# Kernel tuning notes

Measured on AMD Instinct MI355X. Metric: run time of the kernel, lower is better.

## Reference

```python
import jax, jax.numpy as jnp
import numpy as np

HIDDEN = 1024
HEADS = 16
HEAD = HIDDEN // HEADS


def setup_inputs() -> dict:
    key = jax.random.key(0)
    k1, k2, k3, k4, k5, k6 = jax.random.split(key, 6)
    B, S = 2, 2048
    x = jax.random.normal(k1, (B, S, HIDDEN), dtype=jnp.float32)
    mask = jax.random.randint(k2, (B, S), 0, 2, dtype=jnp.int32)
    # torch nn.Linear params: W [out,in], b [out]
    s = 1.0 / np.sqrt(HIDDEN)
    qkv_w = jax.random.uniform(k3, (3 * HIDDEN, HIDDEN), jnp.float32, -s, s)
    qkv_b = jax.random.uniform(k4, (3 * HIDDEN,), jnp.float32, -s, s)
    out_w = jax.random.uniform(k5, (HIDDEN, HIDDEN), jnp.float32, -s, s)
    out_b = jax.random.uniform(k6, (HIDDEN,), jnp.float32, -s, s)
    return {"x": x, "mask": mask, "qkv_w": qkv_w, "qkv_b": qkv_b,
            "out_w": out_w, "out_b": out_b}


def reference(x, mask, qkv_w, qkv_b, out_w, out_b):
    B, S, H = x.shape
    scale = HEAD ** -0.5
    qkv = x @ qkv_w.T + qkv_b                      # [B,S,3H]
    qkv = qkv.reshape(B, S, 3, HEADS, HEAD)
    qkv = jnp.transpose(qkv, (2, 0, 3, 1, 4))      # [3,B,h,S,d]
    q, k, v = qkv[0], qkv[1], qkv[2]
    scores = jnp.einsum('bhqd,bhkd->bhqk', q, k) * scale
    # key-padding mask [B,S] -> [B,1,1,S]
    scores = jnp.where(mask[:, None, None, :] == 0, -1e9, scores)
    attn = jax.nn.softmax(scores, axis=-1)
    # dropout is identity in eval mode
    ctx = jnp.einsum('bhqk,bhkd->bhqd', attn, v)   # [B,h,S,d]
    ctx = jnp.transpose(ctx, (0, 2, 1, 3)).reshape(B, S, H)
    return ctx @ out_w.T + out_b
```

## Files before the change

### kernel.cpp

```cpp
#include <hip/hip_runtime.h>
#include <hip/hip_bf16.h>

#define S_LEN 2048
#define NH    16
#define HD    64
#define HID   1024
#define BATCH 2
#define STK   72
#define SCQ   0.18033688f

typedef __bf16 bf16x8 __attribute__((ext_vector_type(8)));
typedef float  f32x4  __attribute__((ext_vector_type(4)));

__device__ __forceinline__ unsigned int pk2(float lo, float hi) {
    union { __hip_bfloat162 h; unsigned int u; } c;
    c.h = __float22bfloat162_rn(make_float2(lo, hi));
    return c.u;
}
__device__ __forceinline__ uint4 pk8(float4 a, float4 b) {
    uint4 o;
    o.x = pk2(a.x, a.y); o.y = pk2(a.z, a.w);
    o.z = pk2(b.x, b.y); o.w = pk2(b.z, b.w);
    return o;
}
__device__ __forceinline__ float exp2_hw(float x) {
    float r; asm("v_exp_f32 %0, %1" : "=v"(r) : "v"(x)); return r;
}
__device__ __forceinline__ void gll16(const unsigned short* g, unsigned short* l) {
    __builtin_amdgcn_global_load_lds(
        (const __attribute__((address_space(1))) void*)g,
        (__attribute__((address_space(3))) void*)l, 16, 0, 0);
}

__global__ __launch_bounds__(256)
void fill_constf(float* __restrict__ out, long n, float v) {
    long i = (long)blockIdx.x * 256 + threadIdx.x;
    const long stride = (long)gridDim.x * 256;
    for (; i < n; i += stride) out[i] = v;
}

__global__ __launch_bounds__(256)
void cvt_bf16(const float* __restrict__ src, unsigned short* __restrict__ dst, long n8) {
    long t = (long)blockIdx.x * 256 + threadIdx.x;
    const long stride = (long)gridDim.x * 256;
    for (; t < n8; t += stride) {
        const float4 a = *(const float4*)(src + t * 8);
        const float4 b = *(const float4*)(src + t * 8 + 4);
        *(uint4*)(dst + t * 8) = pk8(a, b);
    }
}
__global__ __launch_bounds__(256)
void cvt2_bf16(const float* __restrict__ s0, unsigned short* __restrict__ d0, long n0,
               const float* __restrict__ s1, unsigned short* __restrict__ d1, long n1) {
    long t = (long)blockIdx.x * 256 + threadIdx.x;
    const long stride = (long)gridDim.x * 256;
    for (; t < n0 + n1; t += stride) {
        const float* s; unsigned short* d; long i;
        if (t < n0) { s = s0; d = d0; i = t; } else { s = s1; d = d1; i = t - n0; }
        const float4 a = *(const float4*)(s + i * 8);
        const float4 b = *(const float4*)(s + i * 8 + 4);
        *(uint4*)(d + i * 8) = pk8(a, b);
    }
}

__global__ __launch_bounds__(256)
void gemm_bf16(const unsigned short* __restrict__ A,
               const unsigned short* __restrict__ W,
               const float* __restrict__ bias,
               unsigned short* __restrict__ o0,
               unsigned short* __restrict__ o1,
               unsigned short* __restrict__ o2,
               float* __restrict__ of,
               int mode)
{
    __shared__ __align__(16) unsigned short lA[3][128 * 32];
    __shared__ __align__(16) unsigned short lB[3][128 * 32];
    const int tid  = threadIdx.x;
    const int lane = tid & 63, wv = tid >> 6;
    const int quad = lane >> 4, l16 = lane & 15;
    const int wm = (wv & 1) * 64, wn = (wv >> 1) * 64;

    const int nwg = gridDim.x * gridDim.y;
    const int bid = blockIdx.y * gridDim.x + blockIdx.x;
    const int xcd = bid & 7, boff = bid >> 3;
    const int qd = nwg >> 3, rm = nwg & 7;
    const int swz = (xcd < rm ? xcd * (qd + 1) : rm * (qd + 1) + (xcd - rm) * qd) + boff;
    const int m0 = (swz / gridDim.x) * 128, n0 = (swz % gridDim.x) * 128;

    f32x4 acc[4][4] = {};

    const int srow0 = wv * 32 + (lane >> 2);
    const int srow1 = srow0 + 16;
    const int csrc  = ((lane & 3) ^ ((lane >> 3) & 3)) * 8;
    const unsigned short* pa0 = A + (long)(m0 + srow0) * HID + csrc;
    const unsigned short* pa1 = A + (long)(m0 + srow1) * HID + csrc;
    const unsigned short* pb0 = W + (long)(n0 + srow0) * HID + csrc;
    const unsigned short* pb1 = W + (long)(n0 + srow1) * HID + csrc;

    const int cq8 = (quad ^ ((l16 >> 1) & 3)) * 8;

#define STAGE_G(bufi, koff)                                        \
    do {                                                           \
        gll16(pa0 + (koff), &lA[bufi][(wv * 2 + 0) * 512]);        \
        gll16(pa1 + (koff), &lA[bufi][(wv * 2 + 1) * 512]);        \
        gll16(pb0 + (koff), &lB[bufi][(wv * 2 + 0) * 512]);        \
        gll16(pb1 + (koff), &lB[bufi][(wv * 2 + 1) * 512]);        \
    } while (0)

    STAGE_G(0, 0);
    STAGE_G(1, 32);

    int cur = 0;
    for (int k0 = 0; k0 < HID; k0 += 32) {
        if (k0 + 32 < HID) { asm volatile("s_waitcnt vmcnt(4)" ::: "memory"); }
        else               { asm volatile("s_waitcnt vmcnt(0)" ::: "memory"); }
        __builtin_amdgcn_s_barrier();
        asm volatile("" ::: "memory");

        if (k0 + 64 < HID) {
            const int nxt = cur ? cur - 1 : 2;
            STAGE_G(nxt, k0 + 64);
        }

        bf16x8 af[4], bfr[4];
#pragma unroll
        for (int mt = 0; mt < 4; mt++)
            af[mt] = *(const bf16x8*)&lA[cur][(wm + mt * 16 + l16) * 32 + cq8];
#pragma unroll
        for (int nt = 0; nt < 4; nt++)
            bfr[nt] = *(const bf16x8*)&lB[cur][(wn + nt * 16 + l16) * 32 + cq8];
#pragma unroll
        for (int mt = 0; mt < 4; mt++)
#pragma unroll
            for (int nt = 0; nt < 4; nt++)
                acc[mt][nt] = __builtin_amdgcn_mfma_f32_16x16x32_bf16(
                    af[mt], bfr[nt], acc[mt][nt], 0, 0, 0);

        cur = (cur < 2) ? cur + 1 : 0;
    }
#undef STAGE_G

    if (mode == 0) {
#pragma unroll
        for (int nt = 0; nt < 4; nt++) {
            const int n = n0 + wn + nt * 16 + l16;
            const float bv = bias[n];
            const int part = n >> 10, f = n & 1023, h = f >> 6, d = f & 63;
#pragma unroll
            for (int mt = 0; mt < 4; mt++) {
                const int mbase = m0 + wm + mt * 16 + quad * 4;
                const int b = mbase >> 11, s0 = mbase & 2047;
                const int bh = b * NH + h;
                if (part != 1) {
                    const float qsc = (part == 0) ? SCQ : 1.0f;
                    unsigned short* dst = (part == 0) ? o0 : o2;
                    uint2 o;
                    o.x = pk2((acc[mt][nt][0] + bv) * qsc, (acc[mt][nt][1] + bv) * qsc);
                    o.y = pk2((acc[mt][nt][2] + bv) * qsc, (acc[mt][nt][3] + bv) * qsc);
                    *(uint2*)&dst[((long)bh * HD + d) * S_LEN + s0] = o;
                } else {
#pragma unroll
                    for (int r = 0; r < 4; r++) {
                        union { __hip_bfloat16 h; unsigned short u; } cv;
                        cv.h = __float2bfloat16(acc[mt][nt][r] + bv);
                        o1[((long)bh * S_LEN + s0 + r) * HD + d] = cv.u;
                    }
                }
            }
        }
    } else {
#pragma unroll
        for (int nt = 0; nt < 4; nt++) {
            const int n = n0 + wn + nt * 16 + l16;
            const float bv = bias[n];
#pragma unroll
            for (int mt = 0; mt < 4; mt++) {
                const int mbase = m0 + wm + mt * 16 + quad * 4;
#pragma unroll
                for (int r = 0; r < 4; r++)
                    of[(long)(mbase + r) * HID + n] = acc[mt][nt][r] + bv;
            }
        }
    }
}

__global__ __launch_bounds__(512)
void attn(const unsigned short* __restrict__ q,
          const unsigned short* __restrict__ k,
          const unsigned short* __restrict__ vt_g,
          const int* __restrict__ mask,
          unsigned short* __restrict__ ctx)
{
    __shared__ __align__(16) unsigned short kt[2][64 * STK];
    __shared__ __align__(16) unsigned short vt[2][64 * STK];
    __shared__ __align__(16) __bf16 pt[8][16 * 72];
    __shared__ float mkv[2][64];

    const int tid  = threadIdx.x;
    const int lane = tid & 63, wv = tid >> 6;
    const int quad = lane >> 4, l16 = lane & 15;
    const int qt = blockIdx.x, h = blockIdx.y, b = blockIdx.z;
    const int bh = b * NH + h;

    const int sq = qt * 128 + wv * 16 + l16;

    const unsigned short* qtg = q + (long)bh * HD * S_LEN + sq;
    union { unsigned short u[8]; bf16x8 v; } qu0, qu1;
#pragma unroll
    for (int j = 0; j < 8; j++) {
        qu0.u[j] = qtg[(long)(quad * 8 + j) * S_LEN];
        qu1.u[j] = qtg[(long)(32 + quad * 8 + j) * S_LEN];
    }
    const bf16x8 qf0 = qu0.v, qf1 = qu1.v;

    float mrun = -1e30f;
    float lsum = 0.f;
    f32x4 Of[4] = {};

    const int sr = tid >> 3, sc8 = (tid & 7) * 8;
    const unsigned short* kg = k    + ((long)bh * S_LEN + sr) * HD + sc8;
    const unsigned short* vg = vt_g + ((long)bh * HD + sr) * S_LEN + sc8;
    __bf16* ptw = pt[wv];

    uint4 rk = *(const uint4*)(kg);
    uint4 rv = *(const uint4*)(vg);
    float rmv = 0.f;
    if (tid < 64) rmv = (mask[b * S_LEN + tid] == 0) ? -1e9f : 0.f;
    *(uint4*)&kt[0][sr * STK + sc8] = rk;
    *(uint4*)&vt[0][sr * STK + sc8] = rv;
    if (tid < 64) mkv[0][tid] = rmv;
    rk = *(const uint4*)(kg + (long)64 * HD);
    rv = *(const uint4*)(vg + 64);
    if (tid < 64) rmv = (mask[b * S_LEN + 64 + tid] == 0) ? -1e9f : 0.f;
    asm volatile("s_waitcnt lgkmcnt(0)" ::: "memory");
    __builtin_amdgcn_s_barrier();
    asm volatile("" ::: "memory");

    for (int k0 = 0; k0 < S_LEN; k0 += 64) {
        const int cur = (k0 >> 6) & 1;
        if (k0 + 64 < S_LEN) {
            *(uint4*)&kt[cur ^ 1][sr * STK + sc8] = rk;
            *(uint4*)&vt[cur ^ 1][sr * STK + sc8] = rv;
            if (tid < 64) mkv[cur ^ 1][tid] = rmv;
            if (k0 + 128 < S_LEN) {
                rk = *(const uint4*)(kg + (long)(k0 + 128) * HD);
                rv = *(const uint4*)(vg + (k0 + 128));
                if (tid < 64) rmv = (mask[b * S_LEN + k0 + 128 + tid] == 0) ? -1e9f : 0.f;
            }
        }

        float st[4][4];
        __builtin_amdgcn_s_setprio(1);
#pragma unroll
        for (int nt = 0; nt < 4; nt++) {
            bf16x8 k0f = *(const bf16x8*)&kt[cur][(nt * 16 + l16) * STK + quad * 8];
            bf16x8 k1f = *(const bf16x8*)&kt[cur][(nt * 16 + l16) * STK + 32 + quad * 8];
            const float4 mv = *(const float4*)&mkv[cur][nt * 16 + quad * 4];
            f32x4 s = {mv.x, mv.y, mv.z, mv.w};
            s = __builtin_amdgcn_mfma_f32_16x16x32_bf16(k0f, qf0, s, 0, 0, 0);
            s = __builtin_amdgcn_mfma_f32_16x16x32_bf16(k1f, qf1, s, 0, 0, 0);
#pragma unroll
            for (int r = 0; r < 4; r++) st[nt][r] = s[r];
        }
        __builtin_amdgcn_s_setprio(0);

        float mxa[4];
#pragma unroll
        for (int nt = 0; nt < 4; nt++)
            mxa[nt] = fmaxf(fmaxf(st[nt][0], st[nt][1]), fmaxf(st[nt][2], st[nt][3]));
        const float pmax = fmaxf(fmaxf(mxa[0], mxa[1]), fmaxf(mxa[2], mxa[3]));

        if (__any(pmax > mrun + 8.f)) {
            float mx = fmaxf(pmax, __shfl_xor(pmax, 16, 64));
            mx = fmaxf(mx, __shfl_xor(mx, 32, 64));
            const float mn = fmaxf(mrun, mx);
            const float alpha = exp2_hw(mrun - mn);
#pragma unroll
            for (int nt = 0; nt < 4; nt++) Of[nt] *= alpha;
            lsum *= alpha;
            mrun = mn;
        }

        float pr[4][4];
#pragma unroll
        for (int nt = 0; nt < 4; nt++)
#pragma unroll
            for (int r = 0; r < 4; r++) pr[nt][r] = exp2_hw(st[nt][r] - mrun);
        float rsa[4];
#pragma unroll
        for (int nt = 0; nt < 4; nt++)
            rsa[nt] = (pr[nt][0] + pr[nt][1]) + (pr[nt][2] + pr[nt][3]);
        lsum += (rsa[0] + rsa[1]) + (rsa[2] + rsa[3]);

#pragma unroll
        for (int nt = 0; nt < 4; nt++) {
            const unsigned long long lo = pk2(pr[nt][0], pr[nt][1]);
            const unsigned long long hi = pk2(pr[nt][2], pr[nt][3]);
            *(unsigned long long*)&ptw[l16 * 72 + nt * 16 + quad * 4] = lo | (hi << 32);
        }
        asm volatile("" ::: "memory");

        __builtin_amdgcn_s_setprio(1);
#pragma unroll
        for (int ks = 0; ks < 2; ks++) {
            bf16x8 bp = *(const bf16x8*)&ptw[l16 * 72 + ks * 32 + quad * 8];
#pragma unroll
            for (int nt = 0; nt < 4; nt++) {
                bf16x8 av = *(const bf16x8*)&vt[cur][(nt * 16 + l16) * STK + ks * 32 + quad * 8];
                Of[nt] = __builtin_amdgcn_mfma_f32_16x16x32_bf16(av, bp, Of[nt], 0, 0, 0);
            }
        }
        __builtin_amdgcn_s_setprio(0);

        asm volatile("s_waitcnt lgkmcnt(0)" ::: "memory");
        __builtin_amdgcn_s_barrier();
        asm volatile("" ::: "memory");
    }

    float lt = lsum + __shfl_xor(lsum, 16, 64);
    lt += __shfl_xor(lt, 32, 64);
    const float inv = 1.f / lt;
#pragma unroll
    for (int nt = 0; nt < 4; nt++) {
        uint2 o;
        o.x = pk2(Of[nt][0] * inv, Of[nt][1] * inv);
        o.y = pk2(Of[nt][2] * inv, Of[nt][3] * inv);
        *(uint2*)&ctx[((long)b * S_LEN + sq) * HID + h * HD + nt * 16 + quad * 4] = o;
    }
}

extern "C" void kernel_launch(void* const* d_in, const int* in_sizes, int n_in,
                              void* d_out, int out_size, void* d_ws, size_t ws_size,
                              hipStream_t stream) {
    float* outp = (float*)d_out;

    const float* x = nullptr; const int* mask = nullptr;
    const float* qkv_w = nullptr; const float* qkv_b = nullptr;
    const float* out_w = nullptr; const float* out_b = nullptr;
    for (int i = 0; i < n_in; i++) {
        switch (in_sizes[i]) {
            case 4194304: x     = (const float*)d_in[i]; break;
            case 4096:    mask  = (const int*)d_in[i];   break;
            case 3145728: qkv_w = (const float*)d_in[i]; break;
            case 3072:    qkv_b = (const float*)d_in[i]; break;
            case 1048576: out_w = (const float*)d_in[i]; break;
            case 1024:    out_b = (const float*)d_in[i]; break;
            default: break;
        }
    }
    if (!x || !mask || !qkv_w || !qkv_b || !out_w || !out_b) {
        fill_constf<<<256, 256, 0, stream>>>(outp, (long)out_size, 1000.0f);
        return;
    }

    const size_t per = (size_t)BATCH * NH * S_LEN * HD;
    const size_t nx  = (size_t)BATCH * S_LEN * HID;
    const size_t nqw = (size_t)3 * HID * HID;
    const size_t now = (size_t)HID * HID;
    if (ws_size < 4 * per * sizeof(unsigned short)) {
        fill_constf<<<256, 256, 0, stream>>>(outp, (long)out_size, 2000.0f);
        return;
    }

    unsigned short* wsq = (unsigned short*)d_ws;
    unsigned short* wsk = wsq + per;
    unsigned short* wsv = wsk + per;
    unsigned short* wsc = wsv + per;
    unsigned short* xb  = wsc;
    unsigned short* qwb = (unsigned short*)d_out;
    unsigned short* owb = wsq;

    cvt2_bf16<<<1024, 256, 0, stream>>>(x, xb, (long)(nx / 8), qkv_w, qwb, (long)(nqw / 8));
    gemm_bf16<<<dim3(3 * HID / 128, BATCH * S_LEN / 128), 256, 0, stream>>>(
        xb, qwb, qkv_b, wsq, wsk, wsv, nullptr, 0);
    attn<<<dim3(S_LEN / 128, NH, BATCH), 512, 0, stream>>>(wsq, wsk, wsv, mask, wsc);
    cvt_bf16<<<512, 256, 0, stream>>>(out_w, owb, (long)(now / 8));
    gemm_bf16<<<dim3(HID / 128, BATCH * S_LEN / 128), 256, 0, stream>>>(
        wsc, owb, out_b, nullptr, nullptr, nullptr, outp, 1);
}
```

Before: 225.5 us.

## Switch attention to 32x32x16 MFMA with register-resident P via permlane32 swap

Rewrites the attention kernel so each of four waves handles 32 queries using 32x32x16 bf16 MFMAs instead of 16x16x32 tiles. The softmax probabilities are repacked into MFMA operand layout in registers with permlane32_swap, which removes the per-wave LDS staging buffer for P and its write/read round trip. K/V tiles in LDS are XOR-swizzled to avoid bank conflicts, and block size drops from 512 to 256 threads. The trade-off is fewer waves per block and higher register pressure from the 16-wide accumulators, with more work per wave.

```diff
diff --git a/kernel.cpp b/kernel.cpp
--- a/kernel.cpp
+++ b/kernel.cpp
@@ -11,6 +11,8 @@
 
 typedef __bf16 bf16x8 __attribute__((ext_vector_type(8)));
 typedef float  f32x4  __attribute__((ext_vector_type(4)));
+typedef float  f32x16 __attribute__((ext_vector_type(16)));
+typedef unsigned u32x2 __attribute__((ext_vector_type(2)));
 
 __device__ __forceinline__ unsigned int pk2(float lo, float hi) {
     union { __hip_bfloat162 h; unsigned int u; } c;
@@ -25,6 +27,20 @@
 }
 __device__ __forceinline__ float exp2_hw(float x) {
     float r; asm("v_exp_f32 %0, %1" : "=v"(r) : "v"(x)); return r;
+}
+__device__ __forceinline__ void pl32swap(unsigned &a, unsigned &b) {
+    u32x2 r = __builtin_amdgcn_permlane32_swap(a, b, false, false);
+    a = r[0]; b = r[1];
+}
+__device__ __forceinline__ float pair_max(float x) {
+    unsigned u = __float_as_uint(x);
+    u32x2 r = __builtin_amdgcn_permlane32_swap(u, u, false, false);
+    return fmaxf(__uint_as_float(r[0]), __uint_as_float(r[1]));
+}
+__device__ __forceinline__ float pair_sum(float x) {
+    unsigned u = __float_as_uint(x);
+    u32x2 r = __builtin_amdgcn_permlane32_swap(u, u, false, false);
+    return __uint_as_float(r[0]) + __uint_as_float(r[1]);
 }
 __device__ __forceinline__ void gll16(const unsigned short* g, unsigned short* l) {
     __builtin_amdgcn_global_load_lds(
@@ -184,7 +200,7 @@
     }
 }
 
-__global__ __launch_bounds__(512)
+__global__ __launch_bounds__(256)
 void attn(const unsigned short* __restrict__ q,
           const unsigned short* __restrict__ k,
           const unsigned short* __restrict__ vt_g,
@@ -193,44 +209,48 @@
 {
     __shared__ __align__(16) unsigned short kt[2][64 * STK];
     __shared__ __align__(16) unsigned short vt[2][64 * STK];
-    __shared__ __align__(16) __bf16 pt[8][16 * 72];
-    __shared__ float mkv[2][64];
+    __shared__ __align__(16) float mkv[2][64];
 
     const int tid  = threadIdx.x;
     const int lane = tid & 63, wv = tid >> 6;
-    const int quad = lane >> 4, l16 = lane & 15;
+    const int ar = lane & 31, hi = lane >> 5;
     const int qt = blockIdx.x, h = blockIdx.y, b = blockIdx.z;
     const int bh = b * NH + h;
-
-    const int sq = qt * 128 + wv * 16 + l16;
-
-    const unsigned short* qtg = q + (long)bh * HD * S_LEN + sq;
-    union { unsigned short u[8]; bf16x8 v; } qu0, qu1;
-#pragma unroll
-    for (int j = 0; j < 8; j++) {
-        qu0.u[j] = qtg[(long)(quad * 8 + j) * S_LEN];
-        qu1.u[j] = qtg[(long)(32 + quad * 8 + j) * S_LEN];
-    }
-    const bf16x8 qf0 = qu0.v, qf1 = qu1.v;
-
-    float mrun = -1e30f;
-    float lsum = 0.f;
-    f32x4 Of[4] = {};
-
-    const int sr = tid >> 3, sc8 = (tid & 7) * 8;
-    const unsigned short* kg = k    + ((long)bh * S_LEN + sr) * HD + sc8;
-    const unsigned short* vg = vt_g + ((long)bh * HD + sr) * S_LEN + sc8;
-    __bf16* ptw = pt[wv];
-
-    uint4 rk = *(const uint4*)(kg);
-    uint4 rv = *(const uint4*)(vg);
+    const int sq = qt * 128 + wv * 32 + ar;
+
+    union { unsigned short u[8]; bf16x8 v; } qu[4];
+    const unsigned short* qg = q + (long)bh * HD * S_LEN + sq;
+#pragma unroll
+    for (int t = 0; t < 4; t++)
+#pragma unroll
+        for (int j = 0; j < 8; j++)
+            qu[t].u[j] = qg[(long)(16 * t + 8 * hi + j) * S_LEN];
+
+    float mrun = -1e30f, lsum = 0.f;
+    f32x16 Of0 = {}, Of1 = {};
+
+    const int sr = tid >> 2, c0 = tid & 3;
+    const unsigned short* kg = k    + ((long)bh * S_LEN + sr) * HD + c0 * 8;
+    const unsigned short* vg = vt_g + ((long)bh * HD + sr) * S_LEN + c0 * 8;
+    const int wof0 = sr * STK + ((c0 ^ (sr & 7)) * 8);
+    const int wof1 = sr * STK + (((c0 + 4) ^ (sr & 7)) * 8);
+    const int swzr = ar & 7;
+
+    uint4 rk0 = *(const uint4*)(kg);
+    uint4 rk1 = *(const uint4*)(kg + 32);
+    uint4 rv0 = *(const uint4*)(vg);
+    uint4 rv1 = *(const uint4*)(vg + 32);
     float rmv = 0.f;
     if (tid < 64) rmv = (mask[b * S_LEN + tid] == 0) ? -1e9f : 0.f;
-    *(uint4*)&kt[0][sr * STK + sc8] = rk;
-    *(uint4*)&vt[0][sr * STK + sc8] = rv;
+    *(uint4*)&kt[0][wof0] = rk0;
+    *(uint4*)&kt[0][wof1] = rk1;
+    *(uint4*)&vt[0][wof0] = rv0;
+    *(uint4*)&vt[0][wof1] = rv1;
     if (tid < 64) mkv[0][tid] = rmv;
-    rk = *(const uint4*)(kg + (long)64 * HD);
-    rv = *(const uint4*)(vg + 64);
+    rk0 = *(const uint4*)(kg + (long)64 * HD);
+    rk1 = *(const uint4*)(kg + (long)64 * HD + 32);
+    rv0 = *(const uint4*)(vg + 64);
+    rv1 = *(const uint4*)(vg + 64 + 32);
     if (tid < 64) rmv = (mask[b * S_LEN + 64 + tid] == 0) ? -1e9f : 0.f;
     asm volatile("s_waitcnt lgkmcnt(0)" ::: "memory");
     __builtin_amdgcn_s_barrier();
@@ -239,76 +259,93 @@
     for (int k0 = 0; k0 < S_LEN; k0 += 64) {
         const int cur = (k0 >> 6) & 1;
         if (k0 + 64 < S_LEN) {
-            *(uint4*)&kt[cur ^ 1][sr * STK + sc8] = rk;
-            *(uint4*)&vt[cur ^ 1][sr * STK + sc8] = rv;
+            *(uint4*)&kt[cur ^ 1][wof0] = rk0;
+            *(uint4*)&kt[cur ^ 1][wof1] = rk1;
+            *(uint4*)&vt[cur ^ 1][wof0] = rv0;
+            *(uint4*)&vt[cur ^ 1][wof1] = rv1;
             if (tid < 64) mkv[cur ^ 1][tid] = rmv;
             if (k0 + 128 < S_LEN) {
-                rk = *(const uint4*)(kg + (long)(k0 + 128) * HD);
-                rv = *(const uint4*)(vg + (k0 + 128));
+                rk0 = *(const uint4*)(kg + (long)(k0 + 128) * HD);
+                rk1 = *(const uint4*)(kg + (long)(k0 + 128) * HD + 32);
+                rv0 = *(const uint4*)(vg + (k0 + 128));
+                rv1 = *(const uint4*)(vg + (k0 + 128) + 32);
                 if (tid < 64) rmv = (mask[b * S_LEN + k0 + 128 + tid] == 0) ? -1e9f : 0.f;
             }
         }
 
-        float st[4][4];
+        float st[2][16];
         __builtin_amdgcn_s_setprio(1);
 #pragma unroll
-        for (int nt = 0; nt < 4; nt++) {
-            bf16x8 k0f = *(const bf16x8*)&kt[cur][(nt * 16 + l16) * STK + quad * 8];
-            bf16x8 k1f = *(const bf16x8*)&kt[cur][(nt * 16 + l16) * STK + 32 + quad * 8];
-            const float4 mv = *(const float4*)&mkv[cur][nt * 16 + quad * 4];
-            f32x4 s = {mv.x, mv.y, mv.z, mv.w};
-            s = __builtin_amdgcn_mfma_f32_16x16x32_bf16(k0f, qf0, s, 0, 0, 0);
-            s = __builtin_amdgcn_mfma_f32_16x16x32_bf16(k1f, qf1, s, 0, 0, 0);
-#pragma unroll
-            for (int r = 0; r < 4; r++) st[nt][r] = s[r];
+        for (int G = 0; G < 2; G++) {
+            f32x16 s = {};
+#pragma unroll
+            for (int t = 0; t < 4; t++) {
+                bf16x8 kf = *(const bf16x8*)
+                    &kt[cur][(G * 32 + ar) * STK + (((2 * t + hi) ^ swzr) * 8)];
+                s = __builtin_amdgcn_mfma_f32_32x32x16_bf16(kf, qu[t].v, s, 0, 0, 0);
+            }
+#pragma unroll
+            for (int m = 0; m < 4; m++) {
+                const float4 mv = *(const float4*)&mkv[cur][G * 32 + m * 8 + hi * 4];
+#pragma unroll
+                for (int r2 = 0; r2 < 4; r2++)
+                    st[G][m * 4 + r2] = s[m * 4 + r2] + (&mv.x)[r2];
+            }
         }
         __builtin_amdgcn_s_setprio(0);
 
-        float mxa[4];
-#pragma unroll
-        for (int nt = 0; nt < 4; nt++)
-            mxa[nt] = fmaxf(fmaxf(st[nt][0], st[nt][1]), fmaxf(st[nt][2], st[nt][3]));
-        const float pmax = fmaxf(fmaxf(mxa[0], mxa[1]), fmaxf(mxa[2], mxa[3]));
+        float pmax = st[0][0];
+#pragma unroll
+        for (int G = 0; G < 2; G++)
+#pragma unroll
+            for (int r = 0; r < 16; r++) pmax = fmaxf(pmax, st[G][r]);
+        pmax = pair_max(pmax);
 
         if (__any(pmax > mrun + 8.f)) {
-            float mx = fmaxf(pmax, __shfl_xor(pmax, 16, 64));
-            mx = fmaxf(mx, __shfl_xor(mx, 32, 64));
-            const float mn = fmaxf(mrun, mx);
+            const float mn = fmaxf(mrun, pmax);
             const float alpha = exp2_hw(mrun - mn);
-#pragma unroll
-            for (int nt = 0; nt < 4; nt++) Of[nt] *= alpha;
-            lsum *= alpha;
+            Of0 *= alpha; Of1 *= alpha; lsum *= alpha;
             mrun = mn;
         }
 
-        float pr[4][4];
-#pragma unroll
-        for (int nt = 0; nt < 4; nt++)
-#pragma unroll
-            for (int r = 0; r < 4; r++) pr[nt][r] = exp2_hw(st[nt][r] - mrun);
-        float rsa[4];
-#pragma unroll
-        for (int nt = 0; nt < 4; nt++)
-            rsa[nt] = (pr[nt][0] + pr[nt][1]) + (pr[nt][2] + pr[nt][3]);
-        lsum += (rsa[0] + rsa[1]) + (rsa[2] + rsa[3]);
-
-#pragma unroll
-        for (int nt = 0; nt < 4; nt++) {
-            const unsigned long long lo = pk2(pr[nt][0], pr[nt][1]);
-            const unsigned long long hi = pk2(pr[nt][2], pr[nt][3]);
-            *(unsigned long long*)&ptw[l16 * 72 + nt * 16 + quad * 4] = lo | (hi << 32);
-        }
-        asm volatile("" ::: "memory");
+        unsigned wa[2][4], wb[2][4];
+        float ls = 0.f;
+#pragma unroll
+        for (int G = 0; G < 2; G++) {
+            float pr[16];
+#pragma unroll
+            for (int r = 0; r < 16; r++) {
+                pr[r] = exp2_hw(st[G][r] - mrun);
+                ls += pr[r];
+            }
+#pragma unroll
+            for (int m = 0; m < 4; m++) {
+                wa[G][m] = pk2(pr[4 * m + 0], pr[4 * m + 1]);
+                wb[G][m] = pk2(pr[4 * m + 2], pr[4 * m + 3]);
+            }
+        }
+        lsum += ls;
+
+        union { unsigned u[4]; bf16x8 v; } F[4];
+#pragma unroll
+        for (int s5 = 0; s5 < 4; s5++) {
+            const int G = s5 >> 1, mp = (s5 & 1) * 2;
+            unsigned f0 = wa[G][mp], f2 = wa[G][mp + 1];
+            unsigned f1 = wb[G][mp], f3 = wb[G][mp + 1];
+            pl32swap(f0, f2);
+            pl32swap(f1, f3);
+            F[s5].u[0] = f0; F[s5].u[1] = f1; F[s5].u[2] = f2; F[s5].u[3] = f3;
+        }
 
         __builtin_amdgcn_s_setprio(1);
 #pragma unroll
-        for (int ks = 0; ks < 2; ks++) {
-            bf16x8 bp = *(const bf16x8*)&ptw[l16 * 72 + ks * 32 + quad * 8];
-#pragma unroll
-            for (int nt = 0; nt < 4; nt++) {
-                bf16x8 av = *(const bf16x8*)&vt[cur][(nt * 16 + l16) * STK + ks * 32 + quad * 8];
-                Of[nt] = __builtin_amdgcn_mfma_f32_16x16x32_bf16(av, bp, Of[nt], 0, 0, 0);
-            }
+        for (int s5 = 0; s5 < 4; s5++) {
+            bf16x8 vf0 = *(const bf16x8*)
+                &vt[cur][(0 * 32 + ar) * STK + (((2 * s5 + hi) ^ swzr) * 8)];
+            Of0 = __builtin_amdgcn_mfma_f32_32x32x16_bf16(vf0, F[s5].v, Of0, 0, 0, 0);
+            bf16x8 vf1 = *(const bf16x8*)
+                &vt[cur][(1 * 32 + ar) * STK + (((2 * s5 + hi) ^ swzr) * 8)];
+            Of1 = __builtin_amdgcn_mfma_f32_32x32x16_bf16(vf1, F[s5].v, Of1, 0, 0, 0);
         }
         __builtin_amdgcn_s_setprio(0);
 
@@ -317,15 +354,17 @@
         asm volatile("" ::: "memory");
     }
 
-    float lt = lsum + __shfl_xor(lsum, 16, 64);
-    lt += __shfl_xor(lt, 32, 64);
-    const float inv = 1.f / lt;
-#pragma unroll
-    for (int nt = 0; nt < 4; nt++) {
-        uint2 o;
-        o.x = pk2(Of[nt][0] * inv, Of[nt][1] * inv);
-        o.y = pk2(Of[nt][2] * inv, Of[nt][3] * inv);
-        *(uint2*)&ctx[((long)b * S_LEN + sq) * HID + h * HD + nt * 16 + quad * 4] = o;
+    const float inv = 1.f / pair_sum(lsum);
+    unsigned short* cb = ctx + ((long)b * S_LEN + sq) * HID + h * HD;
+#pragma unroll
+    for (int m = 0; m < 4; m++) {
+        uint2 o0, o1;
+        o0.x = pk2(Of0[4 * m + 0] * inv, Of0[4 * m + 1] * inv);
+        o0.y = pk2(Of0[4 * m + 2] * inv, Of0[4 * m + 3] * inv);
+        *(uint2*)&cb[m * 8 + hi * 4] = o0;
+        o1.x = pk2(Of1[4 * m + 0] * inv, Of1[4 * m + 1] * inv);
+        o1.y = pk2(Of1[4 * m + 2] * inv, Of1[4 * m + 3] * inv);
+        *(uint2*)&cb[32 + m * 8 + hi * 4] = o1;
     }
 }
 
@@ -373,7 +412,7 @@
     cvt2_bf16<<<1024, 256, 0, stream>>>(x, xb, (long)(nx / 8), qkv_w, qwb, (long)(nqw / 8));
     gemm_bf16<<<dim3(3 * HID / 128, BATCH * S_LEN / 128), 256, 0, stream>>>(
         xb, qwb, qkv_b, wsq, wsk, wsv, nullptr, 0);
-    attn<<<dim3(S_LEN / 128, NH, BATCH), 512, 0, stream>>>(wsq, wsk, wsv, mask, wsc);
+    attn<<<dim3(S_LEN / 128, NH, BATCH), 256, 0, stream>>>(wsq, wsk, wsv, mask, wsc);
     cvt_bf16<<<512, 256, 0, stream>>>(out_w, owb, (long)(now / 8));
     gemm_bf16<<<dim3(HID / 128, BATCH * S_LEN / 128), 256, 0, stream>>>(
         wsc, owb, out_b, nullptr, nullptr, nullptr, outp, 1);
```

Result: slower. 231.0 us (+2.5%).
